# Optimization experiments

Hardware: AMD Instinct MI355X
Metric: run time of the kernel (lower is better)

The kernel has to match this reference:

```python
import jax, jax.numpy as jnp
import numpy as np

EPS = 1e-5

def _conv1x1(x, w, b):
    # x: (B,C,H,W), w: (O,C), b: (O,)
    return jnp.einsum('bchw,oc->bohw', x, w) + b[None, :, None, None]

def _maxpool2(x):
    B, C, H, W = x.shape
    return x.reshape(B, C, H // 2, 2, W // 2, 2).max(axis=(3, 5))

def setup_inputs() -> dict:
    key = jax.random.key(0)
    ks = jax.random.split(key, 12)
    B, C, Ci, H, W = 8, 256, 128, 64, 64
    s = lambda k, shape, scale: jax.random.normal(k, shape, jnp.float32) * scale
    return {
        'x': s(ks[0], (B, C, H, W), 1.0),
        'neighborFeat': s(ks[1], (B, C, H, W), 1.0),
        'g_w': s(ks[2], (Ci, C), 0.05), 'g_b': jnp.zeros((Ci,), jnp.float32),
        'theta_w': s(ks[3], (Ci, C), 0.05), 'theta_b': jnp.zeros((Ci,), jnp.float32),
        'phi_w': s(ks[4], (Ci, C), 0.05), 'phi_b': jnp.zeros((Ci,), jnp.float32),
        'w_w': s(ks[5], (C, Ci), 0.05), 'w_b': jnp.zeros((C,), jnp.float32),
        'bn_gamma': s(ks[6], (C,), 0.1) + 1.0,
        'bn_beta': s(ks[7], (C,), 0.1),
        'bn_mean': s(ks[8], (C,), 0.1),
        'bn_var': jax.random.uniform(ks[9], (C,), jnp.float32, 0.5, 1.5),
    }

def reference(x, neighborFeat, g_w, g_b, theta_w, theta_b, phi_w, phi_b,
              w_w, w_b, bn_gamma, bn_beta, bn_mean, bn_var):
    B, C, H, W = x.shape
    Ci = g_w.shape[0]
    # g: conv1x1 on x then maxpool2 -> (B, Nkv, Ci)
    g_x = _maxpool2(_conv1x1(x, g_w, g_b)).reshape(B, Ci, -1).transpose(0, 2, 1)
    # theta: conv1x1 on neighborFeat, full res -> (B, Nq, Ci)
    theta_x = _conv1x1(neighborFeat, theta_w, theta_b).reshape(B, Ci, -1).transpose(0, 2, 1)
    # phi: conv1x1 on neighborFeat then maxpool2 -> (B, Ci, Nkv)
    phi_x = _maxpool2(_conv1x1(neighborFeat, phi_w, phi_b)).reshape(B, Ci, -1)
    f = jnp.einsum('bqc,bck->bqk', theta_x, phi_x)       # (B, Nq, Nkv)
    f_div_C = jax.nn.softmax(f, axis=-1)
    y = jnp.einsum('bqk,bkc->bqc', f_div_C, g_x)          # (B, Nq, Ci)
    y = y.transpose(0, 2, 1).reshape(B, Ci, H, W)
    # W: conv1x1 + BatchNorm (eval mode with running stats)
    wy = _conv1x1(y, w_w, w_b)
    wy = (wy - bn_mean[None, :, None, None]) * (bn_gamma[None, :, None, None]
          * jax.lax.rsqrt(bn_var + EPS)[None, :, None, None]) + bn_beta[None, :, None, None]
    return wy + x
```

## Files before the change

### kernel.cpp

```cpp
#include <hip/hip_runtime.h>

typedef __attribute__((ext_vector_type(8))) short short8;
typedef __attribute__((ext_vector_type(4))) short short4v;
typedef __attribute__((ext_vector_type(4))) float f32x4;
typedef __attribute__((ext_vector_type(16))) float f32x16;
typedef __attribute__((ext_vector_type(4))) unsigned u32x4;

__device__ __forceinline__ float bf2f(short s) {
  union { unsigned u; float f; } cv;
  cv.u = ((unsigned)(unsigned short)s) << 16;
  return cv.f;
}
__device__ __forceinline__ short f2bf(float f) {
  union { float f; unsigned u; } cv;
  cv.f = f;
  unsigned r = (cv.u + 0x7fffu + ((cv.u >> 16) & 1u)) >> 16;
  return (short)(unsigned short)r;
}
__device__ __forceinline__ unsigned cvtpk(float a, float b) {
  unsigned r;
  asm("v_cvt_pk_bf16_f32 %0, %1, %2" : "=v"(r) : "v"(a), "v"(b));
  return r;
}
__device__ __forceinline__ void load_lds16(const void* g, void* l) {
  __builtin_amdgcn_global_load_lds(
      (const __attribute__((address_space(1))) void*)g,
      (__attribute__((address_space(3))) void*)l, 16, 0, 0);
}

#define MFMA16(a, b, c) __builtin_amdgcn_mfma_f32_16x16x32_bf16((a), (b), (c), 0, 0, 0)
#define MFMA32(a, b, c) __builtin_amdgcn_mfma_f32_32x32x16_bf16((a), (b), (c), 0, 0, 0)

__global__ __launch_bounds__(256) void cvt_w(
    const float* __restrict__ s0, const float* __restrict__ s1,
    const float* __restrict__ s2, const float* __restrict__ s3,
    short* __restrict__ d)
{
  const float* srcs[4] = {s0, s1, s2, s3};
  const float* s = srcs[blockIdx.y];
  int i = (blockIdx.x * 256 + threadIdx.x) * 4;
  f32x4 v = *reinterpret_cast<const f32x4*>(s + i);
  short4v o;
  #pragma unroll
  for (int j = 0; j < 4; j++) o[j] = f2bf(v[j]);
  *reinterpret_cast<short4v*>(d + (size_t)blockIdx.y * 32768 + i) = o;
}

template <int NPROJ, int MODE1>
__device__ __forceinline__ void conv_body(
    short (*in_t)[40], short (*wt)[40],
    const float* __restrict__ in,
    const short* __restrict__ w0, const float* __restrict__ bias0,
    const short* __restrict__ w1, const float* __restrict__ bias1,
    short* __restrict__ out0, short* __restrict__ out1)
{
  const int b = blockIdx.y;
  const int p0 = blockIdx.x * 128;
  const int tid = threadIdx.x;
  const int wave = tid >> 6, lane = tid & 63;
  const int lr = lane & 15, lg = lane >> 4;

  const short* wsrc[2] = {w0, w1};

  f32x4 acc[NPROJ][8];
  #pragma unroll
  for (int pj = 0; pj < NPROJ; pj++)
    #pragma unroll
    for (int n = 0; n < 8; n++) acc[pj][n] = (f32x4)0.0f;

  for (int kc = 0; kc < 256; kc += 32) {
    __syncthreads();
    {
      int c = tid >> 4;
      int pg = (tid & 15) * 8;
      const float* src = in + ((size_t)(b * 256 + kc + c)) * 4096 + p0 + pg;
      f32x4 v0 = *reinterpret_cast<const f32x4*>(src);
      f32x4 v1 = *reinterpret_cast<const f32x4*>(src + 4);
      #pragma unroll
      for (int j = 0; j < 8; j++) {
        int p = pg + j;
        int a = ((p & 63) >> 1) * 4 + ((p >> 6) << 1) + (p & 1);
        float fv = (j < 4) ? v0[j] : v1[j - 4];
        in_t[a][c ^ ((((a >> 3) & 3)) << 3)] = f2bf(fv);
      }
    }
    if (tid < NPROJ * 128) {
      int pj = tid >> 7, o = tid & 127;
      const short8* src = reinterpret_cast<const short8*>(wsrc[pj] + (size_t)o * 256 + kc);
      int f = (o >> 3) & 3;
      #pragma unroll
      for (int gq = 0; gq < 4; gq++)
        *reinterpret_cast<short8*>(&wt[pj * 128 + o][(gq ^ f) * 8]) = src[gq];
    }
    __syncthreads();

    int arow = wave * 16 + lr;
    short8 afrag = *reinterpret_cast<const short8*>(
        &in_t[arow][(lg ^ ((arow >> 3) & 3)) * 8]);
    #pragma unroll
    for (int pj = 0; pj < NPROJ; pj++) {
      #pragma unroll
      for (int n = 0; n < 8; n++) {
        int brow = n * 16 + lr;
        short8 bfrag = *reinterpret_cast<const short8*>(
            &wt[pj * 128 + brow][(lg ^ ((brow >> 3) & 3)) * 8]);
        acc[pj][n] = MFMA16(afrag, bfrag, acc[pj][n]);
      }
    }
  }

  const float* bsrc[2] = {bias0, bias1};
  short* osrc[2] = {out0, out1};
  const int kp = blockIdx.x * 32 + wave * 4 + lg;
  #pragma unroll
  for (int pj = 0; pj < NPROJ; pj++) {
    const int mode = (pj == 0 && NPROJ == 2) ? 0 : MODE1;
    #pragma unroll
    for (int n = 0; n < 8; n++) {
      int o = n * 16 + lr;
      float bv = bsrc[pj][o];
      if (mode == 0) {
        #pragma unroll
        for (int r = 0; r < 4; r++) {
          int pix = (wave * 4 + lg) * 2 + (r & 1) + ((r >> 1) & 1) * 64;
          osrc[pj][((size_t)b * 4096 + p0 + pix) * 128 + o] = f2bf(acc[pj][n][r] + bv);
        }
      } else {
        f32x4 v = acc[pj][n];
        float pv = fmaxf(fmaxf(v[0], v[1]), fmaxf(v[2], v[3])) + bv;
        if (mode == 1)
          osrc[pj][((size_t)b * 1024 + kp) * 128 + o] = f2bf(pv);
        else
          osrc[pj][((size_t)b * 128 + o) * 1024 + kp] = f2bf(pv);
      }
    }
  }
}

__global__ __launch_bounds__(512, 4) void conv_all(
    const float* __restrict__ nb, const float* __restrict__ x,
    const short* __restrict__ th_w, const float* __restrict__ th_b,
    const short* __restrict__ ph_w, const float* __restrict__ ph_b,
    const short* __restrict__ g_w, const float* __restrict__ g_b,
    short* __restrict__ theta, short* __restrict__ phi_kc,
    short* __restrict__ g_ck)
{
  __shared__ short in_t[128][40];
  __shared__ short wt[256][40];
  if (blockIdx.z == 0)
    conv_body<2, 1>(in_t, wt, nb, th_w, th_b, ph_w, ph_b, theta, phi_kc);
  else
    conv_body<1, 2>(in_t, wt, x, g_w, g_b, nullptr, nullptr, g_ck, nullptr);
}

__global__ __launch_bounds__(512) void attn(
    const short* __restrict__ theta, const short* __restrict__ phi,
    const short* __restrict__ g, short* __restrict__ y)
{
  __shared__ char lds[131072];
  __shared__ float ml[8][32][2];

  const int b = blockIdx.y;
  const int q0 = blockIdx.x * 128;
  const int tid = threadIdx.x;
  const int wave = tid >> 6, lane = tid & 63;
  const int l31 = lane & 31, hi = lane >> 5;
  const int zw = wave >> 2, wq = wave & 3;

  short8 ath[8];
  {
    const short* tq = theta + ((size_t)b * 4096 + q0 + wq * 32 + l31) * 128 + hi * 8;
    #pragma unroll
    for (int s = 0; s < 8; s++)
      ath[s] = *reinterpret_cast<const short8*>(tq + s * 16);
  }

  const short* psrc[4];
  {
    int rb = wq * 16 + (lane >> 4), sl = lane & 15;
    #pragma unroll
    for (int i = 0; i < 4; i++) {
      int r = rb + i * 4;
      psrc[i] = phi + ((size_t)b * 1024 + zw * 512 + r) * 128 + ((sl ^ (r & 15)) * 8);
    }
  }
  const short* gsrc[4];
  {
    int rb = wq * 32 + (lane >> 3), sl = lane & 7;
    #pragma unroll
    for (int i = 0; i < 4; i++) {
      int r = rb + i * 8;
      gsrc[i] = g + ((size_t)b * 128 + r) * 1024 + zw * 512 + ((sl ^ (r & 7)) * 8);
    }
  }

  float mrun = -1e30f, lpart = 0.0f;
  f32x16 acc[4];
  #pragma unroll
  for (int n = 0; n < 4; n++) acc[n] = (f32x16)0.0f;

  {
    char* pb = lds + zw * 16384 + wq * 4096;
    char* gb = lds + 65536 + zw * 16384 + wq * 4096;
    #pragma unroll
    for (int i = 0; i < 4; i++) {
      load_lds16(psrc[i], pb + i * 1024);
      load_lds16(gsrc[i], gb + i * 1024);
    }
  }

  for (int t = 0; t < 8; t++) {
    __syncthreads();
    char* pb = lds + ((t & 1) * 2 + zw) * 16384;
    char* gb = lds + 65536 + ((t & 1) * 2 + zw) * 16384;

    if (t < 7) {
      char* pb2 = lds + (((t + 1) & 1) * 2 + zw) * 16384 + wq * 4096;
      char* gb2 = lds + 65536 + (((t + 1) & 1) * 2 + zw) * 16384 + wq * 4096;
      #pragma unroll
      for (int i = 0; i < 4; i++) {
        load_lds16(psrc[i] + (t + 1) * 8192, pb2 + i * 1024);
        load_lds16(gsrc[i] + (t + 1) * 64, gb2 + i * 1024);
      }
    }

    f32x16 facc0 = (f32x16)0.0f, facc1 = (f32x16)0.0f;
    __builtin_amdgcn_s_setprio(1);
    #pragma unroll
    for (int s = 0; s < 8; s++) {
      int slot = (s << 1) | hi;
      short8 pf0 = *reinterpret_cast<const short8*>(
          pb + l31 * 256 + ((slot ^ (l31 & 15)) * 16));
      short8 pf1 = *reinterpret_cast<const short8*>(
          pb + (32 + l31) * 256 + ((slot ^ (l31 & 15)) * 16));
      facc0 = MFMA32(pf0, ath[s], facc0);
      facc1 = MFMA32(pf1, ath[s], facc1);
    }
    __builtin_amdgcn_s_setprio(0);

    float mv[16];
    #pragma unroll
    for (int r = 0; r < 16; r++) mv[r] = fmaxf(facc0[r], facc1[r]);
    #pragma unroll
    for (int s = 8; s >= 1; s >>= 1)
      #pragma unroll
      for (int r = 0; r < s; r++) mv[r] = fmaxf(mv[r], mv[r + s]);
    float m = fmaxf(mv[0], __shfl_xor(mv[0], 32));

    if (__any(m - mrun > 10.0f)) {
      float mn = fmaxf(mrun, m);
      float sc = __expf(mrun - mn);
      mrun = mn;
      lpart *= sc;
      #pragma unroll
      for (int reg = 0; reg < 16; reg++) {
        int qr = (reg & 3) + 8 * (reg >> 2) + 4 * hi;
        float sr = __shfl(sc, qr);
        #pragma unroll
        for (int n = 0; n < 4; n++) acc[n][reg] *= sr;
      }
    }
    #pragma unroll
    for (int r = 0; r < 16; r++) facc0[r] = __expf(facc0[r] - mrun);
    #pragma unroll
    for (int r = 0; r < 16; r++) facc1[r] = __expf(facc1[r] - mrun);
    {
      float sv[16];
      #pragma unroll
      for (int r = 0; r < 16; r++) sv[r] = facc0[r] + facc1[r];
      #pragma unroll
      for (int s = 8; s >= 1; s >>= 1)
        #pragma unroll
        for (int r = 0; r < s; r++) sv[r] += sv[r + s];
      lpart += sv[0];
    }

    __builtin_amdgcn_s_setprio(1);
    #pragma unroll
    for (int s = 0; s < 4; s++) {
      const int base = (s & 1) * 8;
      float p0, p1, p2, p3, p4, p5, p6, p7;
      if (s < 2) {
        p0 = facc0[base + 0]; p1 = facc0[base + 1]; p2 = facc0[base + 2]; p3 = facc0[base + 3];
        p4 = facc0[base + 4]; p5 = facc0[base + 5]; p6 = facc0[base + 6]; p7 = facc0[base + 7];
      } else {
        p0 = facc1[base + 0]; p1 = facc1[base + 1]; p2 = facc1[base + 2]; p3 = facc1[base + 3];
        p4 = facc1[base + 4]; p5 = facc1[base + 5]; p6 = facc1[base + 6]; p7 = facc1[base + 7];
      }
      unsigned P0w0 = cvtpk(p0, p1), P0w1 = cvtpk(p2, p3);
      unsigned P1w0 = cvtpk(p4, p5), P1w1 = cvtpk(p6, p7);
      unsigned x0 = (unsigned)__shfl_xor((int)P0w0, 32);
      unsigned x1 = (unsigned)__shfl_xor((int)P0w1, 32);
      unsigned y0 = (unsigned)__shfl_xor((int)P1w0, 32);
      unsigned y1 = (unsigned)__shfl_xor((int)P1w1, 32);
      union { u32x4 u; short8 s8; } pf;
      pf.u[0] = hi ? y0 : P0w0;
      pf.u[1] = hi ? y1 : P0w1;
      pf.u[2] = hi ? P1w0 : x0;
      pf.u[3] = hi ? P1w1 : x1;
      int slot = (s << 1) | hi;
      #pragma unroll
      for (int n = 0; n < 4; n++) {
        int rg = n * 32 + l31;
        short8 gf = *reinterpret_cast<const short8*>(
            gb + rg * 128 + ((slot ^ (rg & 7)) * 16));
        acc[n] = MFMA32(pf.s8, gf, acc[n]);
      }
    }
    __builtin_amdgcn_s_setprio(0);
  }

  float lsum = lpart + __shfl_xor(lpart, 32);
  if (lane < 32) { ml[wave][l31][0] = mrun; ml[wave][l31][1] = lsum; }
  __syncthreads();
  float mo = ml[wave ^ 4][l31][0];
  float lo = ml[wave ^ 4][l31][1];
  float M = fmaxf(mrun, mo);
  float e0 = __expf(mrun - M), e1 = __expf(mo - M);
  float wown = e0 / (e0 * lsum + e1 * lo);
  #pragma unroll
  for (int reg = 0; reg < 16; reg++) {
    int qr = (reg & 3) + 8 * (reg >> 2) + 4 * hi;
    float wr = __shfl(wown, qr);
    #pragma unroll
    for (int n = 0; n < 4; n++) acc[n][reg] *= wr;
  }
  float* mb = (float*)(lds + wq * 16384);
  if (zw == 1) {
    #pragma unroll
    for (int n = 0; n < 4; n++)
      #pragma unroll
      for (int reg = 0; reg < 16; reg++) {
        int qrow = (reg & 3) + 8 * (reg >> 2) + 4 * hi;
        mb[qrow * 128 + n * 32 + l31] = acc[n][reg];
      }
  }
  __syncthreads();
  if (zw == 0) {
    #pragma unroll
    for (int n = 0; n < 4; n++)
      #pragma unroll
      for (int reg = 0; reg < 16; reg++) {
        int qrow = (reg & 3) + 8 * (reg >> 2) + 4 * hi;
        float v = acc[n][reg] + mb[qrow * 128 + n * 32 + l31];
        y[((size_t)b * 4096 + q0 + wq * 32 + qrow) * 128 + n * 32 + l31] = f2bf(v);
      }
  }
}

__global__ __launch_bounds__(512) void wconv_bn(
    const short* __restrict__ yb, const short* __restrict__ ww,
    const float* __restrict__ wb,
    const float* __restrict__ gamma, const float* __restrict__ beta,
    const float* __restrict__ mean, const float* __restrict__ var,
    const float* __restrict__ x, float* __restrict__ out)
{
  __shared__ short y_s[128][136];
  __shared__ float sc_s[256];
  __shared__ float sh_s[256];

  const int b = blockIdx.y;
  const int q0 = blockIdx.x * 128;
  const int tid = threadIdx.x;
  const int wave = tid >> 6, lane = tid & 63;
  const int lr = lane & 15, lg = lane >> 4;

  {
    int r = tid >> 2, c0 = (tid & 3) * 32;
    const short8* src = reinterpret_cast<const short8*>(
        yb + ((size_t)(b * 4096 + q0 + r)) * 128 + c0);
    short8* dst = reinterpret_cast<short8*>(&y_s[r][c0]);
    #pragma unroll
    for (int j = 0; j < 4; j++) dst[j] = src[j];
    if (tid < 256) {
      float s = gamma[tid] * rsqrtf(var[tid] + 1e-5f);
      sc_s[tid] = s;
      sh_s[tid] = (wb[tid] - mean[tid]) * s + beta[tid];
    }
  }
  __syncthreads();

  f32x4 acc[2][8];
  #pragma unroll
  for (int m = 0; m < 2; m++)
    #pragma unroll
    for (int n = 0; n < 8; n++) acc[m][n] = (f32x4)0.0f;

  #pragma unroll
  for (int kk = 0; kk < 4; kk++) {
    short8 af[2], bfr[8];
    #pragma unroll
    for (int m = 0; m < 2; m++)
      af[m] = *reinterpret_cast<const short8*>(
          ww + (size_t)(wave * 32 + m * 16 + lr) * 128 + kk * 32 + lg * 8);
    #pragma unroll
    for (int n = 0; n < 8; n++)
      bfr[n] = *reinterpret_cast<const short8*>(&y_s[n * 16 + lr][kk * 32 + lg * 8]);
    #pragma unroll
    for (int m = 0; m < 2; m++)
      #pragma unroll
      for (int n = 0; n < 8; n++)
        acc[m][n] = MFMA16(af[m], bfr[n], acc[m][n]);
  }

  #pragma unroll
  for (int m = 0; m < 2; m++) {
    #pragma unroll
    for (int n = 0; n < 8; n++) {
      #pragma unroll
      for (int r = 0; r < 4; r++) {
        int co = wave * 32 + m * 16 + lg * 4 + r;
        int q = q0 + n * 16 + lr;
        size_t oidx = ((size_t)b * 256 + co) * 4096 + q;
        float v = acc[m][n][r] * sc_s[co] + sh_s[co];
        out[oidx] = v + x[oidx];
      }
    }
  }
}

extern "C" void kernel_launch(void* const* d_in, const int* in_sizes, int n_in,
                              void* d_out, int out_size, void* d_ws, size_t ws_size,
                              hipStream_t stream)
{
  const float* x    = (const float*)d_in[0];
  const float* nb   = (const float*)d_in[1];
  const float* g_w  = (const float*)d_in[2];
  const float* g_b  = (const float*)d_in[3];
  const float* th_w = (const float*)d_in[4];
  const float* th_b = (const float*)d_in[5];
  const float* ph_w = (const float*)d_in[6];
  const float* ph_b = (const float*)d_in[7];
  const float* w_w  = (const float*)d_in[8];
  const float* w_b  = (const float*)d_in[9];
  const float* gam  = (const float*)d_in[10];
  const float* bet  = (const float*)d_in[11];
  const float* mu   = (const float*)d_in[12];
  const float* var  = (const float*)d_in[13];
  float* out = (float*)d_out;

  char* ws = (char*)d_ws;
  short* theta_full = (short*)(ws);
  short* yb         = (short*)(ws + (size_t)(8u << 20));
  short* phi_kc     = (short*)(ws + (size_t)(16u << 20));
  short* g_ck       = (short*)(ws + (size_t)(18u << 20));
  short* wts        = (short*)(ws + (size_t)(20u << 20));
  short* th_wb = wts;
  short* ph_wb = wts + 32768;
  short* g_wb  = wts + 2 * 32768;
  short* w_wb  = wts + 3 * 32768;

  cvt_w<<<dim3(32, 4), 256, 0, stream>>>(th_w, ph_w, g_w, w_w, wts);
  conv_all<<<dim3(32, 8, 2), 512, 0, stream>>>(nb, x, th_wb, th_b, ph_wb, ph_b,
                                               g_wb, g_b, theta_full, phi_kc, g_ck);
  attn<<<dim3(32, 8), 512, 0, stream>>>(theta_full, phi_kc, g_ck, yb);
  wconv_bn<<<dim3(32, 8), 512, 0, stream>>>(yb, w_wb, w_b, gam, bet, mu, var, x, out);
}
```

Baseline: 82.38 us.

## Fuse W-conv+BN into attention epilogue and use exp2 with pre-scaled theta

The attention kernel now writes its normalized y tile into shared memory and runs the W 1x1 conv, BatchNorm and residual add in the same block. This removes the separate wconv_bn launch and the bf16 y round trip through global memory. Theta is also pre-multiplied by log2(e) in the conv epilogue, so the softmax can use the raw v_exp_f32 (exp2) instruction instead of __expf. The rescale threshold is raised to match the log2 domain. The cost is extra shared-memory reuse and register pressure in the already heavy attention kernel.

```diff
diff --git a/kernel.cpp b/kernel.cpp
--- a/kernel.cpp
+++ b/kernel.cpp
@@ -6,6 +6,8 @@
 typedef __attribute__((ext_vector_type(16))) float f32x16;
 typedef __attribute__((ext_vector_type(4))) unsigned u32x4;
 
+#define LOG2E 1.4426950408889634f
+
 __device__ __forceinline__ float bf2f(short s) {
   union { unsigned u; float f; } cv;
   cv.u = ((unsigned)(unsigned short)s) << 16;
@@ -20,6 +22,11 @@
 __device__ __forceinline__ unsigned cvtpk(float a, float b) {
   unsigned r;
   asm("v_cvt_pk_bf16_f32 %0, %1, %2" : "=v"(r) : "v"(a), "v"(b));
+  return r;
+}
+__device__ __forceinline__ float fexp2(float x) {
+  float r;
+  asm("v_exp_f32 %0, %1" : "=v"(r) : "v"(x));
   return r;
 }
 __device__ __forceinline__ void load_lds16(const void* g, void* l) {
@@ -123,7 +130,8 @@
         #pragma unroll
         for (int r = 0; r < 4; r++) {
           int pix = (wave * 4 + lg) * 2 + (r & 1) + ((r >> 1) & 1) * 64;
-          osrc[pj][((size_t)b * 4096 + p0 + pix) * 128 + o] = f2bf(acc[pj][n][r] + bv);
+          osrc[pj][((size_t)b * 4096 + p0 + pix) * 128 + o] =
+              f2bf((acc[pj][n][r] + bv) * LOG2E);
         }
       } else {
         f32x4 v = acc[pj][n];
@@ -153,9 +161,13 @@
     conv_body<1, 2>(in_t, wt, x, g_w, g_b, nullptr, nullptr, g_ck, nullptr);
 }
 
-__global__ __launch_bounds__(512) void attn(
+__global__ __launch_bounds__(512) void attn_wconv(
     const short* __restrict__ theta, const short* __restrict__ phi,
-    const short* __restrict__ g, short* __restrict__ y)
+    const short* __restrict__ g, const short* __restrict__ ww,
+    const float* __restrict__ wb,
+    const float* __restrict__ gamma, const float* __restrict__ beta,
+    const float* __restrict__ mean, const float* __restrict__ var,
+    const float* __restrict__ x, float* __restrict__ out)
 {
   __shared__ char lds[131072];
   __shared__ float ml[8][32][2];
@@ -247,9 +259,9 @@
       for (int r = 0; r < s; r++) mv[r] = fmaxf(mv[r], mv[r + s]);
     float m = fmaxf(mv[0], __shfl_xor(mv[0], 32));
 
-    if (__any(m - mrun > 10.0f)) {
+    if (__any(m - mrun > 14.0f)) {
       float mn = fmaxf(mrun, m);
-      float sc = __expf(mrun - mn);
+      float sc = fexp2(mrun - mn);
       mrun = mn;
       lpart *= sc;
       #pragma unroll
@@ -261,9 +273,9 @@
       }
     }
     #pragma unroll
-    for (int r = 0; r < 16; r++) facc0[r] = __expf(facc0[r] - mrun);
-    #pragma unroll
-    for (int r = 0; r < 16; r++) facc1[r] = __expf(facc1[r] - mrun);
+    for (int r = 0; r < 16; r++) facc0[r] = fexp2(facc0[r] - mrun);
+    #pragma unroll
+    for (int r = 0; r < 16; r++) facc1[r] = fexp2(facc1[r] - mrun);
     {
       float sv[16];
       #pragma unroll
@@ -313,10 +325,19 @@
   float lsum = lpart + __shfl_xor(lpart, 32);
   if (lane < 32) { ml[wave][l31][0] = mrun; ml[wave][l31][1] = lsum; }
   __syncthreads();
+
+  float* sc_s = (float*)(lds + 114688);
+  float* sh_s = (float*)(lds + 118784);
+  if (tid < 256) {
+    float s = gamma[tid] * rsqrtf(var[tid] + 1e-5f);
+    sc_s[tid] = s;
+    sh_s[tid] = (wb[tid] - mean[tid]) * s + beta[tid];
+  }
+
   float mo = ml[wave ^ 4][l31][0];
   float lo = ml[wave ^ 4][l31][1];
   float M = fmaxf(mrun, mo);
-  float e0 = __expf(mrun - M), e1 = __expf(mo - M);
+  float e0 = fexp2(mrun - M), e1 = fexp2(mo - M);
   float wown = e0 / (e0 * lsum + e1 * lo);
   #pragma unroll
   for (int reg = 0; reg < 16; reg++) {
@@ -336,6 +357,7 @@
       }
   }
   __syncthreads();
+  short* y_s = (short*)(lds + 65536);
   if (zw == 0) {
     #pragma unroll
     for (int n = 0; n < 4; n++)
@@ -343,76 +365,46 @@
       for (int reg = 0; reg < 16; reg++) {
         int qrow = (reg & 3) + 8 * (reg >> 2) + 4 * hi;
         float v = acc[n][reg] + mb[qrow * 128 + n * 32 + l31];
-        y[((size_t)b * 4096 + q0 + wq * 32 + qrow) * 128 + n * 32 + l31] = f2bf(v);
-      }
-  }
-}
-
-__global__ __launch_bounds__(512) void wconv_bn(
-    const short* __restrict__ yb, const short* __restrict__ ww,
-    const float* __restrict__ wb,
-    const float* __restrict__ gamma, const float* __restrict__ beta,
-    const float* __restrict__ mean, const float* __restrict__ var,
-    const float* __restrict__ x, float* __restrict__ out)
-{
-  __shared__ short y_s[128][136];
-  __shared__ float sc_s[256];
-  __shared__ float sh_s[256];
-
-  const int b = blockIdx.y;
-  const int q0 = blockIdx.x * 128;
-  const int tid = threadIdx.x;
-  const int wave = tid >> 6, lane = tid & 63;
+        y_s[(wq * 32 + qrow) * 136 + n * 32 + l31] = f2bf(v);
+      }
+  }
+  __syncthreads();
+
   const int lr = lane & 15, lg = lane >> 4;
-
-  {
-    int r = tid >> 2, c0 = (tid & 3) * 32;
-    const short8* src = reinterpret_cast<const short8*>(
-        yb + ((size_t)(b * 4096 + q0 + r)) * 128 + c0);
-    short8* dst = reinterpret_cast<short8*>(&y_s[r][c0]);
-    #pragma unroll
-    for (int j = 0; j < 4; j++) dst[j] = src[j];
-    if (tid < 256) {
-      float s = gamma[tid] * rsqrtf(var[tid] + 1e-5f);
-      sc_s[tid] = s;
-      sh_s[tid] = (wb[tid] - mean[tid]) * s + beta[tid];
-    }
-  }
-  __syncthreads();
-
-  f32x4 acc[2][8];
-  #pragma unroll
-  for (int m = 0; m < 2; m++)
-    #pragma unroll
-    for (int n = 0; n < 8; n++) acc[m][n] = (f32x4)0.0f;
+  f32x4 acc2[2][8];
+  #pragma unroll
+  for (int mm = 0; mm < 2; mm++)
+    #pragma unroll
+    for (int n = 0; n < 8; n++) acc2[mm][n] = (f32x4)0.0f;
 
   #pragma unroll
   for (int kk = 0; kk < 4; kk++) {
     short8 af[2], bfr[8];
     #pragma unroll
-    for (int m = 0; m < 2; m++)
-      af[m] = *reinterpret_cast<const short8*>(
-          ww + (size_t)(wave * 32 + m * 16 + lr) * 128 + kk * 32 + lg * 8);
+    for (int mm = 0; mm < 2; mm++)
+      af[mm] = *reinterpret_cast<const short8*>(
+          ww + (size_t)(wave * 32 + mm * 16 + lr) * 128 + kk * 32 + lg * 8);
     #pragma unroll
     for (int n = 0; n < 8; n++)
-      bfr[n] = *reinterpret_cast<const short8*>(&y_s[n * 16 + lr][kk * 32 + lg * 8]);
-    #pragma unroll
-    for (int m = 0; m < 2; m++)
+      bfr[n] = *reinterpret_cast<const short8*>(
+          &y_s[(n * 16 + lr) * 136 + kk * 32 + lg * 8]);
+    #pragma unroll
+    for (int mm = 0; mm < 2; mm++)
       #pragma unroll
       for (int n = 0; n < 8; n++)
-        acc[m][n] = MFMA16(af[m], bfr[n], acc[m][n]);
-  }
-
-  #pragma unroll
-  for (int m = 0; m < 2; m++) {
+        acc2[mm][n] = MFMA16(af[mm], bfr[n], acc2[mm][n]);
+  }
+
+  #pragma unroll
+  for (int mm = 0; mm < 2; mm++) {
     #pragma unroll
     for (int n = 0; n < 8; n++) {
       #pragma unroll
       for (int r = 0; r < 4; r++) {
-        int co = wave * 32 + m * 16 + lg * 4 + r;
+        int co = wave * 32 + mm * 16 + lg * 4 + r;
         int q = q0 + n * 16 + lr;
         size_t oidx = ((size_t)b * 256 + co) * 4096 + q;
-        float v = acc[m][n][r] * sc_s[co] + sh_s[co];
+        float v = acc2[mm][n][r] * sc_s[co] + sh_s[co];
         out[oidx] = v + x[oidx];
       }
     }
@@ -441,10 +433,9 @@
 
   char* ws = (char*)d_ws;
   short* theta_full = (short*)(ws);
-  short* yb         = (short*)(ws + (size_t)(8u << 20));
-  short* phi_kc     = (short*)(ws + (size_t)(16u << 20));
-  short* g_ck       = (short*)(ws + (size_t)(18u << 20));
-  short* wts        = (short*)(ws + (size_t)(20u << 20));
+  short* phi_kc     = (short*)(ws + (size_t)(8u << 20));
+  short* g_ck       = (short*)(ws + (size_t)(10u << 20));
+  short* wts        = (short*)(ws + (size_t)(12u << 20));
   short* th_wb = wts;
   short* ph_wb = wts + 32768;
   short* g_wb  = wts + 2 * 32768;
@@ -453,6 +444,6 @@
   cvt_w<<<dim3(32, 4), 256, 0, stream>>>(th_w, ph_w, g_w, w_w, wts);
   conv_all<<<dim3(32, 8, 2), 512, 0, stream>>>(nb, x, th_wb, th_b, ph_wb, ph_b,
                                                g_wb, g_b, theta_full, phi_kc, g_ck);
-  attn<<<dim3(32, 8), 512, 0, stream>>>(theta_full, phi_kc, g_ck, yb);
-  wconv_bn<<<dim3(32, 8), 512, 0, stream>>>(yb, w_wb, w_b, gam, bet, mu, var, x, out);
-}
+  attn_wconv<<<dim3(32, 8), 512, 0, stream>>>(theta_full, phi_kc, g_ck, w_wb, w_b,
+                                              gam, bet, mu, var, x, out);
+}
```

Result: faster. 74.68 us (median of 3 runs) (-9.4%).
